# Optimization experiments

Measured on AMD Instinct MI355X. Metric: run time of the kernel, lower is better.

Reference implementation:

```python
import jax, jax.numpy as jnp
import numpy as np

EPS = 1e-5

def _bn_relu(z, gamma, beta):
    # BatchNorm1d (training mode: biased batch stats) + ReLU, per-feature over batch dim
    mean = jnp.mean(z, axis=0)
    var = jnp.var(z, axis=0)  # biased, matches torch BN normalization
    zn = (z - mean) * jax.lax.rsqrt(var + EPS) * gamma + beta
    return jax.nn.relu(zn)


def setup_inputs() -> dict:
    key = jax.random.key(0)
    ks = jax.random.split(key, 16)
    N, D_IN, H, D_OUT = 2097152, 16, 32, 1
    def lin(kw, kb, fan_in, fan_out):
        bound = 1.0 / np.sqrt(fan_in)
        W = jax.random.uniform(kw, (fan_out, fan_in), jnp.float32, -bound, bound)
        b = jax.random.uniform(kb, (fan_out,), jnp.float32, -bound, bound)
        return W, b
    W1, b1 = lin(ks[0], ks[1], D_IN, H)
    W2, b2 = lin(ks[2], ks[3], H, H)
    W3, b3 = lin(ks[4], ks[5], H, H)
    W4, b4 = lin(ks[6], ks[7], H, D_OUT)
    x = jax.random.normal(ks[8], (N, D_IN), jnp.float32)
    return {
        "x": x,
        "W1": W1, "b1": b1, "g1": jnp.ones((H,), jnp.float32), "be1": jnp.zeros((H,), jnp.float32),
        "W2": W2, "b2": b2, "g2": jnp.ones((H,), jnp.float32), "be2": jnp.zeros((H,), jnp.float32),
        "W3": W3, "b3": b3, "g3": jnp.ones((H,), jnp.float32), "be3": jnp.zeros((H,), jnp.float32),
        "W4": W4, "b4": b4,
    }


def reference(x, W1, b1, g1, be1, W2, b2, g2, be2, W3, b3, g3, be3, W4, b4):
    p1 = _bn_relu(x @ W1.T + b1, g1, be1)    # [N, H]
    p2 = _bn_relu(p1 @ W2.T + b2, g2, be2)   # [N, H]
    p3 = _bn_relu(p2 @ W3.T + b3, g3, be3)   # [N, H]
    return p3 @ W4.T + b4                    # [N, 1]
```

## Files before the change

### kernel.cpp

```cpp
#include <hip/hip_runtime.h>

#define EPS 1e-5f
#define NTHR 256
#define NBLK 1024
#define NSLOT 8

typedef __bf16 bf16x8 __attribute__((ext_vector_type(8)));
typedef float f32x16 __attribute__((ext_vector_type(16)));


template<int DEPTH>
__global__ __launch_bounds__(NTHR) void k_fwd(
    const float* __restrict__ x, __bf16* __restrict__ xb,
    const float* __restrict__ W1, const float* __restrict__ b1,
    const float* __restrict__ g1, const float* __restrict__ be1,
    const float* __restrict__ W2, const float* __restrict__ b2,
    const float* __restrict__ g2, const float* __restrict__ be2,
    const float* __restrict__ W3, const float* __restrict__ b3,
    const float* __restrict__ g3, const float* __restrict__ be3,
    const float* __restrict__ W4, const float* __restrict__ b4,
    float* __restrict__ stats, float* __restrict__ out, int N)
{
    constexpr bool STATS = (DEPTH < 4);
    __shared__ float s_stat[3][64];
    __shared__ float s_a[3][32];
    __shared__ float s_e[3][32];
    __shared__ float s_b[64];

    const int tid = threadIdx.x;
    const float invN = 1.0f / (float)N;

    if (tid < 64) {
        for (int L = 0; L < DEPTH - 1; ++L) {
            float a = 0.f;
            #pragma unroll
            for (int s = 0; s < NSLOT; ++s) a += stats[L * (NSLOT * 64) + s * 64 + tid];
            s_stat[L][tid] = a;
        }
    }
    __syncthreads();
    if (tid < 32) {
        const float* gs[3]  = {g1, g2, g3};
        const float* bes[3] = {be1, be2, be3};
        const float* bs[3]  = {b1, b2, b3};
        for (int L = 0; L < DEPTH - 1; ++L) {
            float mu = s_stat[L][tid] * invN;
            float v  = s_stat[L][32 + tid] * invN - mu * mu;
            float a  = gs[L][tid] * rsqrtf(v + EPS);
            s_a[L][tid] = a;
            s_e[L][tid] = bs[L][tid] - mu + bes[L][tid] / a;
        }
    }
    if (STATS && tid < 64) s_b[tid] = 0.f;
    __syncthreads();

    const int lane = tid & 63;
    const int h = lane >> 5;
    const int ml = lane & 31;

    bf16x8 w1f;
    {
        const float* p = W1 + ml * 16 + h * 8;
        #pragma unroll
        for (int j = 0; j < 8; ++j) w1f[j] = (__bf16)p[j];
    }
    bf16x8 w2f0 = {}, w2f1 = {}, w3f0 = {}, w3f1 = {};
    if (DEPTH >= 2) {
        #pragma unroll
        for (int kh = 0; kh < 2; ++kh)
            #pragma unroll
            for (int j = 0; j < 8; ++j) {
                int pk = (j & 3) + 8 * (j >> 2) + 4 * h + 16 * kh;
                float v = W2[ml * 32 + pk] * s_a[0][pk];
                if (kh == 0) w2f0[j] = (__bf16)v; else w2f1[j] = (__bf16)v;
            }
    }
    if (DEPTH >= 3) {
        #pragma unroll
        for (int kh = 0; kh < 2; ++kh)
            #pragma unroll
            for (int j = 0; j < 8; ++j) {
                int pk = (j & 3) + 8 * (j >> 2) + 4 * h + 16 * kh;
                float v = W3[ml * 32 + pk] * s_a[1][pk];
                if (kh == 0) w3f0[j] = (__bf16)v; else w3f1[j] = (__bf16)v;
            }
    }

    f32x16 c1, c2 = {}, c3 = {};
    float w4c[16];
    #pragma unroll
    for (int i = 0; i < 16; ++i) {
        int p = (i & 3) + 8 * (i >> 2) + 4 * h;
        c1[i] = (DEPTH == 1) ? b1[p] : s_e[0][p];
        if (DEPTH >= 2) c2[i] = (DEPTH == 2) ? b2[p] : s_e[1][p];
        if (DEPTH >= 3) c3[i] = (DEPTH == 3) ? b3[p] : s_e[2][p];
        if (DEPTH == 4) w4c[i] = W4[p] * s_a[2][p]; else w4c[i] = 0.f;
    }
    const float b4v = (DEPTH == 4) ? b4[0] : 0.f;

    const int ntiles = N >> 5;
    const int nwaves = gridDim.x * (NTHR / 64);
    const int gwave  = blockIdx.x * (NTHR / 64) + (tid >> 6);

    float sums[16], sqs[16];
    #pragma unroll
    for (int i = 0; i < 16; ++i) { sums[i] = 0.f; sqs[i] = 0.f; }

    auto loadx = [&](int t) -> bf16x8 {
        if (DEPTH == 1) {
            int row = (t << 5) + ml;
            const float4* xp = (const float4*)(x + (size_t)row * 16 + h * 8);
            float4 u0 = xp[0], u1 = xp[1];
            bf16x8 xf;
            xf[0] = (__bf16)u0.x; xf[1] = (__bf16)u0.y; xf[2] = (__bf16)u0.z; xf[3] = (__bf16)u0.w;
            xf[4] = (__bf16)u1.x; xf[5] = (__bf16)u1.y; xf[6] = (__bf16)u1.z; xf[7] = (__bf16)u1.w;
            *(bf16x8*)(xb + ((size_t)t * 64 + lane) * 8) = xf;
            return xf;
        } else {
            return *(const bf16x8*)(xb + ((size_t)t * 64 + lane) * 8);
        }
    };

    auto tile = [&](int t, bf16x8 xf) {
        f32x16 a1 = __builtin_amdgcn_mfma_f32_32x32x16_bf16(w1f, xf, c1, 0, 0, 0);
        if (DEPTH == 1) {
            #pragma unroll
            for (int i = 0; i < 16; ++i) { sums[i] += a1[i]; sqs[i] = fmaf(a1[i], a1[i], sqs[i]); }
            return;
        }
        bf16x8 qa, qb;
        #pragma unroll
        for (int j = 0; j < 8; ++j) {
            qa[j] = (__bf16)fmaxf(a1[j], 0.f);
            qb[j] = (__bf16)fmaxf(a1[8 + j], 0.f);
        }
        f32x16 a2 = __builtin_amdgcn_mfma_f32_32x32x16_bf16(w2f0, qa, c2, 0, 0, 0);
        a2 = __builtin_amdgcn_mfma_f32_32x32x16_bf16(w2f1, qb, a2, 0, 0, 0);
        if (DEPTH == 2) {
            #pragma unroll
            for (int i = 0; i < 16; ++i) { sums[i] += a2[i]; sqs[i] = fmaf(a2[i], a2[i], sqs[i]); }
            return;
        }
        bf16x8 pa, pb;
        #pragma unroll
        for (int j = 0; j < 8; ++j) {
            pa[j] = (__bf16)fmaxf(a2[j], 0.f);
            pb[j] = (__bf16)fmaxf(a2[8 + j], 0.f);
        }
        f32x16 a3 = __builtin_amdgcn_mfma_f32_32x32x16_bf16(w3f0, pa, c3, 0, 0, 0);
        a3 = __builtin_amdgcn_mfma_f32_32x32x16_bf16(w3f1, pb, a3, 0, 0, 0);
        if (DEPTH == 3) {
            #pragma unroll
            for (int i = 0; i < 16; ++i) { sums[i] += a3[i]; sqs[i] = fmaf(a3[i], a3[i], sqs[i]); }
            return;
        }
        float o = 0.f;
        #pragma unroll
        for (int i = 0; i < 16; ++i) o = fmaf(w4c[i], fmaxf(a3[i], 0.f), o);
        o += __shfl_xor(o, 32);
        if (h == 0) out[(t << 5) + ml] = o + b4v;
    };

    int t = gwave;
    for (; t + nwaves < ntiles; t += 2 * nwaves) {
        bf16x8 x0 = loadx(t);
        bf16x8 x1 = loadx(t + nwaves);
        tile(t, x0);
        tile(t + nwaves, x1);
    }
    if (t < ntiles) {
        bf16x8 x0 = loadx(t);
        tile(t, x0);
    }

    if (STATS) {
        #pragma unroll
        for (int i = 0; i < 16; ++i) {
            float s = sums[i], q = sqs[i];
            #pragma unroll
            for (int d = 1; d <= 16; d <<= 1) {
                s += __shfl_xor(s, d);
                q += __shfl_xor(q, d);
            }
            if (ml == 0) {
                int p = (i & 3) + 8 * (i >> 2) + 4 * h;
                atomicAdd(&s_b[p], s);
                atomicAdd(&s_b[32 + p], q);
            }
        }
        __syncthreads();
        if (tid < 64) {
            int L = DEPTH - 1;
            atomicAdd(&stats[L * (NSLOT * 64) + (blockIdx.x & (NSLOT - 1)) * 64 + tid], s_b[tid]);
        }
    }
}

extern "C" void kernel_launch(void* const* d_in, const int* in_sizes, int n_in,
                              void* d_out, int out_size, void* d_ws, size_t ws_size,
                              hipStream_t stream) {
    const float* x   = (const float*)d_in[0];
    const float* W1  = (const float*)d_in[1];
    const float* b1  = (const float*)d_in[2];
    const float* g1  = (const float*)d_in[3];
    const float* be1 = (const float*)d_in[4];
    const float* W2  = (const float*)d_in[5];
    const float* b2  = (const float*)d_in[6];
    const float* g2  = (const float*)d_in[7];
    const float* be2 = (const float*)d_in[8];
    const float* W3  = (const float*)d_in[9];
    const float* b3  = (const float*)d_in[10];
    const float* g3  = (const float*)d_in[11];
    const float* be3 = (const float*)d_in[12];
    const float* W4  = (const float*)d_in[13];
    const float* b4  = (const float*)d_in[14];
    float* out = (float*)d_out;
    int N = in_sizes[0] / 16;

    __bf16* xb   = (__bf16*)d_ws;
    float* stats = (float*)((char*)d_ws + (size_t)N * 16 * 2);

    hipMemsetAsync(stats, 0, 3 * NSLOT * 64 * sizeof(float), stream);

    k_fwd<1><<<NBLK, NTHR, 0, stream>>>(x, xb, W1, b1, g1, be1, W2, b2, g2, be2, W3, b3, g3, be3, W4, b4, stats, out, N);
    k_fwd<2><<<NBLK, NTHR, 0, stream>>>(x, xb, W1, b1, g1, be1, W2, b2, g2, be2, W3, b3, g3, be3, W4, b4, stats, out, N);
    k_fwd<3><<<NBLK, NTHR, 0, stream>>>(x, xb, W1, b1, g1, be1, W2, b2, g2, be2, W3, b3, g3, be3, W4, b4, stats, out, N);
    k_fwd<4><<<NBLK, NTHR, 0, stream>>>(x, xb, W1, b1, g1, be1, W2, b2, g2, be2, W3, b3, g3, be3, W4, b4, stats, out, N);
}
```

Before: 321.6 us.

## Give each wave a contiguous tile range, unroll loads by four, reduce stats via per-wave shared slots

Each wave now handles a contiguous block of tiles instead of a grid-stride interleave, and the loop issues four tiles' loads before computing them. This aims for more memory-level parallelism and better locality in the streaming passes. The block-level stats reduction swaps shared-memory atomics for per-wave shared slots summed by one thread group, and the global atomic slots are doubled to cut contention. Contiguous per-wave ranges may hurt DRAM channel spread compared with interleaved access, and more values held in flight raises register pressure.

```diff
diff --git a/kernel.cpp b/kernel.cpp
--- a/kernel.cpp
+++ b/kernel.cpp
@@ -3,7 +3,7 @@
 #define EPS 1e-5f
 #define NTHR 256
 #define NBLK 1024
-#define NSLOT 8
+#define NSLOT 16
 
 typedef __bf16 bf16x8 __attribute__((ext_vector_type(8)));
 typedef float f32x16 __attribute__((ext_vector_type(16)));
@@ -25,7 +25,7 @@
     __shared__ float s_stat[3][64];
     __shared__ float s_a[3][32];
     __shared__ float s_e[3][32];
-    __shared__ float s_b[64];
+    __shared__ float s_w[NTHR / 64][64];
 
     const int tid = threadIdx.x;
     const float invN = 1.0f / (float)N;
@@ -51,7 +51,6 @@
             s_e[L][tid] = bs[L][tid] - mu + bes[L][tid] / a;
         }
     }
-    if (STATS && tid < 64) s_b[tid] = 0.f;
     __syncthreads();
 
     const int lane = tid & 63;
@@ -99,27 +98,16 @@
     const float b4v = (DEPTH == 4) ? b4[0] : 0.f;
 
     const int ntiles = N >> 5;
-    const int nwaves = gridDim.x * (NTHR / 64);
+    const int nwaves = NBLK * (NTHR / 64);
     const int gwave  = blockIdx.x * (NTHR / 64) + (tid >> 6);
+    const int tpw    = ntiles / nwaves;
+    const int rem    = ntiles - tpw * nwaves;
+    const int t0     = gwave * tpw + (gwave < rem ? gwave : rem);
+    const int cnt    = tpw + (gwave < rem ? 1 : 0);
 
     float sums[16], sqs[16];
     #pragma unroll
     for (int i = 0; i < 16; ++i) { sums[i] = 0.f; sqs[i] = 0.f; }
-
-    auto loadx = [&](int t) -> bf16x8 {
-        if (DEPTH == 1) {
-            int row = (t << 5) + ml;
-            const float4* xp = (const float4*)(x + (size_t)row * 16 + h * 8);
-            float4 u0 = xp[0], u1 = xp[1];
-            bf16x8 xf;
-            xf[0] = (__bf16)u0.x; xf[1] = (__bf16)u0.y; xf[2] = (__bf16)u0.z; xf[3] = (__bf16)u0.w;
-            xf[4] = (__bf16)u1.x; xf[5] = (__bf16)u1.y; xf[6] = (__bf16)u1.z; xf[7] = (__bf16)u1.w;
-            *(bf16x8*)(xb + ((size_t)t * 64 + lane) * 8) = xf;
-            return xf;
-        } else {
-            return *(const bf16x8*)(xb + ((size_t)t * 64 + lane) * 8);
-        }
-    };
 
     auto tile = [&](int t, bf16x8 xf) {
         f32x16 a1 = __builtin_amdgcn_mfma_f32_32x32x16_bf16(w1f, xf, c1, 0, 0, 0);
@@ -161,19 +149,63 @@
         if (h == 0) out[(t << 5) + ml] = o + b4v;
     };
 
-    int t = gwave;
-    for (; t + nwaves < ntiles; t += 2 * nwaves) {
-        bf16x8 x0 = loadx(t);
-        bf16x8 x1 = loadx(t + nwaves);
-        tile(t, x0);
-        tile(t + nwaves, x1);
-    }
-    if (t < ntiles) {
-        bf16x8 x0 = loadx(t);
-        tile(t, x0);
+    auto cvt = [&](float4 a, float4 b) -> bf16x8 {
+        bf16x8 xf;
+        xf[0] = (__bf16)a.x; xf[1] = (__bf16)a.y; xf[2] = (__bf16)a.z; xf[3] = (__bf16)a.w;
+        xf[4] = (__bf16)b.x; xf[5] = (__bf16)b.y; xf[6] = (__bf16)b.z; xf[7] = (__bf16)b.w;
+        return xf;
+    };
+
+    const int nb4 = cnt & ~3;
+    if (DEPTH == 1) {
+        for (int i0 = 0; i0 < nb4; i0 += 4) {
+            const float* base = x + (size_t)((t0 + i0) << 5) * 16;
+            const float4* p0 = (const float4*)(base + (size_t)(ml)      * 16 + h * 8);
+            const float4* p1 = (const float4*)(base + (size_t)(32 + ml) * 16 + h * 8);
+            const float4* p2 = (const float4*)(base + (size_t)(64 + ml) * 16 + h * 8);
+            const float4* p3 = (const float4*)(base + (size_t)(96 + ml) * 16 + h * 8);
+            float4 a0 = p0[0], b0 = p0[1];
+            float4 a1 = p1[0], b1_ = p1[1];
+            float4 a2 = p2[0], b2_ = p2[1];
+            float4 a3 = p3[0], b3_ = p3[1];
+            bf16x8 x0 = cvt(a0, b0), x1 = cvt(a1, b1_), x2 = cvt(a2, b2_), x3 = cvt(a3, b3_);
+            __bf16* w = xb + ((size_t)(t0 + i0) * 64 + lane) * 8;
+            *(bf16x8*)(w)        = x0;
+            *(bf16x8*)(w + 512)  = x1;
+            *(bf16x8*)(w + 1024) = x2;
+            *(bf16x8*)(w + 1536) = x3;
+            tile(t0 + i0,     x0);
+            tile(t0 + i0 + 1, x1);
+            tile(t0 + i0 + 2, x2);
+            tile(t0 + i0 + 3, x3);
+        }
+        for (int i = nb4; i < cnt; ++i) {
+            int row = ((t0 + i) << 5) + ml;
+            const float4* xp = (const float4*)(x + (size_t)row * 16 + h * 8);
+            bf16x8 xf = cvt(xp[0], xp[1]);
+            *(bf16x8*)(xb + ((size_t)(t0 + i) * 64 + lane) * 8) = xf;
+            tile(t0 + i, xf);
+        }
+    } else {
+        for (int i0 = 0; i0 < nb4; i0 += 4) {
+            const __bf16* r = xb + ((size_t)(t0 + i0) * 64 + lane) * 8;
+            bf16x8 x0 = *(const bf16x8*)(r);
+            bf16x8 x1 = *(const bf16x8*)(r + 512);
+            bf16x8 x2 = *(const bf16x8*)(r + 1024);
+            bf16x8 x3 = *(const bf16x8*)(r + 1536);
+            tile(t0 + i0,     x0);
+            tile(t0 + i0 + 1, x1);
+            tile(t0 + i0 + 2, x2);
+            tile(t0 + i0 + 3, x3);
+        }
+        for (int i = nb4; i < cnt; ++i) {
+            bf16x8 xf = *(const bf16x8*)(xb + ((size_t)(t0 + i) * 64 + lane) * 8);
+            tile(t0 + i, xf);
+        }
     }
 
     if (STATS) {
+        const int wid = tid >> 6;
         #pragma unroll
         for (int i = 0; i < 16; ++i) {
             float s = sums[i], q = sqs[i];
@@ -184,14 +216,15 @@
             }
             if (ml == 0) {
                 int p = (i & 3) + 8 * (i >> 2) + 4 * h;
-                atomicAdd(&s_b[p], s);
-                atomicAdd(&s_b[32 + p], q);
+                s_w[wid][p] = s;
+                s_w[wid][32 + p] = q;
             }
         }
         __syncthreads();
         if (tid < 64) {
+            float a = s_w[0][tid] + s_w[1][tid] + s_w[2][tid] + s_w[3][tid];
             int L = DEPTH - 1;
-            atomicAdd(&stats[L * (NSLOT * 64) + (blockIdx.x & (NSLOT - 1)) * 64 + tid], s_b[tid]);
+            atomicAdd(&stats[L * (NSLOT * 64) + (blockIdx.x & (NSLOT - 1)) * 64 + tid], a);
         }
     }
 }
```

After: 314.9 us. 2.1% less time.
